# Kernel tuning notes

Hardware: AMD Instinct MI355X
Metric: run time of the kernel (lower is better)

Reference implementation:

```python
import jax, jax.numpy as jnp
import numpy as np

B, C, H, W = 32, 17, 96, 72
K = 3
DIL = 1
PAD = (K // 2) * DIL
KK = K * K


def setup_inputs() -> dict:
    key = jax.random.key(0)
    k1, k2, k3, k4, k5 = jax.random.split(key, 5)
    x = jax.random.normal(k1, (B, C, H, W), jnp.float32)
    offsets = jax.random.normal(k2, (B, 2 * C * KK, H, W), jnp.float32)
    mask = jax.random.uniform(k3, (B, C * KK, H, W), jnp.float32)
    # depthwise conv: weight [C_out=C, C_in/groups=1, K, K], bias [C]
    weight = jax.random.normal(k4, (C, 1, K, K), jnp.float32) * 0.1
    bias = jax.random.normal(k5, (C,), jnp.float32) * 0.01
    return {"x": x, "offsets": offsets, "mask": mask, "weight": weight, "bias": bias}


def _deform_conv(x, offsets, mask, weight, bias):
    # Modulated deformable conv (DCNv2), depthwise, offset_groups == channels.
    off = offsets.reshape(B, C, KK, 2, H, W)
    dy = off[:, :, :, 0]  # [B,C,KK,H,W]
    dx = off[:, :, :, 1]
    m = mask.reshape(B, C, KK, H, W)

    ky, kx = jnp.meshgrid(jnp.arange(K), jnp.arange(K), indexing="ij")
    ky = ky.reshape(KK)
    kx = kx.reshape(KK)
    hh = jnp.arange(H)
    ww = jnp.arange(W)
    # base sampling grid [KK,H,W]
    base_y = (-PAD + ky[:, None, None] * DIL + hh[None, :, None] + 0 * ww[None, None, :]).astype(jnp.float32)
    base_x = (-PAD + kx[:, None, None] * DIL + 0 * hh[None, :, None] + ww[None, None, :]).astype(jnp.float32)

    py = base_y[None, None] + dy  # [B,C,KK,H,W]
    px = base_x[None, None] + dx

    y0f = jnp.floor(py)
    x0f = jnp.floor(px)
    wy = py - y0f
    wx = px - x0f
    y0 = y0f.astype(jnp.int32)
    x0 = x0f.astype(jnp.int32)

    img = x.reshape(B, C, H * W)

    def corner(yi, xi, w):
        # zero-padding semantics: out-of-bounds corners contribute 0
        valid = (yi >= 0) & (yi < H) & (xi >= 0) & (xi < W)
        idx = jnp.clip(yi, 0, H - 1) * W + jnp.clip(xi, 0, W - 1)
        v = jnp.take_along_axis(img, idx.reshape(B, C, -1), axis=2).reshape(B, C, KK, H, W)
        return v * jnp.where(valid, w, 0.0)

    val = (corner(y0, x0, (1 - wy) * (1 - wx))
           + corner(y0, x0 + 1, (1 - wy) * wx)
           + corner(y0 + 1, x0, wy * (1 - wx))
           + corner(y0 + 1, x0 + 1, wy * wx))

    out = jnp.einsum("bckhw,ck->bchw", val * m, weight.reshape(C, KK))
    return out + bias[None, :, None, None]


def reference(x, offsets, mask, weight, bias):
    return _deform_conv(x, offsets, mask, weight, bias)
```

## Files before the change

kernel.cpp:

```cpp
#include <hip/hip_runtime.h>

#define Bn   32
#define Cn   17
#define Hn   96
#define Wn   72
#define Kn   3
#define KKn  9
#define PADn 1
#define HWn  (Hn * Wn)
#define TPB  576
#define ROWS_PER_BLOCK 32
#define NBLK_X (Hn / ROWS_PER_BLOCK)
#define NPX  4

#define PSTR 75
#define PROWS 99
#define XS_SIZE (PROWS * PSTR)

__global__ __launch_bounds__(TPB) void deform_conv_kernel(
    const float* __restrict__ x,
    const float* __restrict__ offsets,
    const float* __restrict__ mask,
    const float* __restrict__ weight,
    const float* __restrict__ bias,
    float* __restrict__ out)
{
    __shared__ float xs[XS_SIZE];

    const int tid = threadIdx.x;
    const int bc  = blockIdx.y;
    const int c   = bc % Cn;

    for (int i = tid; i < XS_SIZE; i += TPB) xs[i] = 0.f;
    __syncthreads();

    {
        const float4* __restrict__ xp4 = (const float4*)(x + (size_t)bc * HWn);
        #pragma unroll
        for (int j = 0; j < HWn / 4 / TPB; ++j) {
            const int ci  = j * TPB + tid;
            const float4 v = xp4[ci];
            const int idx = ci * 4;
            const int y = idx / Wn;
            const int xcol = idx - y * Wn;
            float* d = &xs[(y + 1) * PSTR + (xcol + 1)];
            d[0] = v.x; d[1] = v.y; d[2] = v.z; d[3] = v.w;
        }
    }
    __syncthreads();

    const int w  = tid % Wn;
    const int h0 = blockIdx.x * ROWS_PER_BLOCK + tid / Wn;
    const int hw0 = h0 * Wn + w;

    const float* __restrict__ offp = offsets + (size_t)bc * (KKn * 2 * HWn);
    const float* __restrict__ mp   = mask    + (size_t)bc * (KKn * HWn);
    const float* __restrict__ wp   = weight  + c * KKn;

    const float bv = bias[c];
    float acc[NPX] = {bv, bv, bv, bv};

    const float wf = (float)w;
    float hpf[NPX];
    #pragma unroll
    for (int p = 0; p < NPX; ++p) hpf[p] = (float)(h0 + 8 * p);

    #pragma unroll
    for (int kk = 0; kk < KKn; ++kk) {
        const float wk  = wp[kk];
        const int   ky  = kk / Kn;
        const int   kx  = kk - ky * Kn;
        const float kyo = (float)(ky - PADn);
        const float kxo = (float)(kx - PADn);

        float dyv[NPX], dxv[NPX], mv[NPX];
        #pragma unroll
        for (int p = 0; p < NPX; ++p) {
            const int hw_p = hw0 + p * 8 * Wn;
            dyv[p] = offp[(size_t)(kk * 2 + 0) * HWn + hw_p];
            dxv[p] = offp[(size_t)(kk * 2 + 1) * HWn + hw_p];
            mv[p]  = mp[(size_t)kk * HWn + hw_p];
        }

        #pragma unroll
        for (int p = 0; p < NPX; ++p) {
            float py = hpf[p] + (dyv[p] + kyo);
            float px = wf     + (dxv[p] + kxo);
            py = fminf(fmaxf(py, -1.f), (float)Hn);
            px = fminf(fmaxf(px, -1.f), (float)Wn);

            const float y0f = floorf(py);
            const float x0f = floorf(px);
            const float wy  = py - y0f;
            const float wx  = px - x0f;
            const int y0 = (int)y0f;
            const int x0 = (int)x0f;

            const float* pr = &xs[(y0 + 1) * PSTR + (x0 + 1)];
            const float v00 = pr[0];
            const float v01 = pr[1];
            const float v10 = pr[PSTR];
            const float v11 = pr[PSTR + 1];

            const float top = v00 + wx * (v01 - v00);
            const float bot = v10 + wx * (v11 - v10);
            const float v   = top + wy * (bot - top);

            acc[p] += v * (mv[p] * wk);
        }
    }

    const size_t ob = (size_t)bc * HWn;
    #pragma unroll
    for (int p = 0; p < NPX; ++p)
        out[ob + hw0 + p * 8 * Wn] = acc[p];
}

extern "C" void kernel_launch(void* const* d_in, const int* in_sizes, int n_in,
                              void* d_out, int out_size, void* d_ws, size_t ws_size,
                              hipStream_t stream) {
    const float* x       = (const float*)d_in[0];
    const float* offsets = (const float*)d_in[1];
    const float* mask    = (const float*)d_in[2];
    const float* weight  = (const float*)d_in[3];
    const float* bias    = (const float*)d_in[4];
    float* out = (float*)d_out;

    dim3 block(TPB, 1, 1);
    dim3 grid(NBLK_X, Bn * Cn, 1);
    deform_conv_kernel<<<grid, block, 0, stream>>>(x, offsets, mask, weight, bias, out);
}
```

Measured before the change: 449.3 us.

## Vectorize per-thread pixel loads with float4 nontemporal accesses and border-only zeroing

```diff
diff --git a/kernel.cpp b/kernel.cpp
--- a/kernel.cpp
+++ b/kernel.cpp
@@ -9,13 +9,15 @@
 #define PADn 1
 #define HWn  (Hn * Wn)
 #define TPB  576
-#define ROWS_PER_BLOCK 32
-#define NBLK_X (Hn / ROWS_PER_BLOCK)
 #define NPX  4
+#define CHUNK (TPB * NPX)
+#define NBLK_X (HWn / CHUNK)
 
 #define PSTR 75
 #define PROWS 99
 #define XS_SIZE (PROWS * PSTR)
+
+typedef float f4 __attribute__((ext_vector_type(4)));
 
 __global__ __launch_bounds__(TPB) void deform_conv_kernel(
     const float* __restrict__ x,
@@ -31,15 +33,23 @@
     const int bc  = blockIdx.y;
     const int c   = bc % Cn;
 
-    for (int i = tid; i < XS_SIZE; i += TPB) xs[i] = 0.f;
-    __syncthreads();
+    if (tid < 225) {
+        const int r  = (tid < 75) ? 0 : ((tid < 150) ? 97 : 98);
+        xs[r * PSTR + (tid % 75)] = 0.f;
+    } else if (tid < 513) {
+        const int i  = tid - 225;
+        const int r  = 1 + i / 3;
+        const int j  = i % 3;
+        const int cc = (j == 0) ? 0 : (72 + j);
+        xs[r * PSTR + cc] = 0.f;
+    }
 
     {
-        const float4* __restrict__ xp4 = (const float4*)(x + (size_t)bc * HWn);
+        const f4* __restrict__ xp4 = (const f4*)(x + (size_t)bc * HWn);
         #pragma unroll
         for (int j = 0; j < HWn / 4 / TPB; ++j) {
             const int ci  = j * TPB + tid;
-            const float4 v = xp4[ci];
+            const f4 v = xp4[ci];
             const int idx = ci * 4;
             const int y = idx / Wn;
             const int xcol = idx - y * Wn;
@@ -49,9 +59,9 @@
     }
     __syncthreads();
 
-    const int w  = tid % Wn;
-    const int h0 = blockIdx.x * ROWS_PER_BLOCK + tid / Wn;
-    const int hw0 = h0 * Wn + w;
+    const int hw0 = blockIdx.x * CHUNK + tid * NPX;
+    const int h   = hw0 / Wn;
+    const int w0  = hw0 - h * Wn;
 
     const float* __restrict__ offp = offsets + (size_t)bc * (KKn * 2 * HWn);
     const float* __restrict__ mp   = mask    + (size_t)bc * (KKn * HWn);
@@ -60,10 +70,8 @@
     const float bv = bias[c];
     float acc[NPX] = {bv, bv, bv, bv};
 
-    const float wf = (float)w;
-    float hpf[NPX];
-    #pragma unroll
-    for (int p = 0; p < NPX; ++p) hpf[p] = (float)(h0 + 8 * p);
+    const float hf  = (float)h;
+    const float wf0 = (float)w0;
 
     #pragma unroll
     for (int kk = 0; kk < KKn; ++kk) {
@@ -73,19 +81,23 @@
         const float kyo = (float)(ky - PADn);
         const float kxo = (float)(kx - PADn);
 
-        float dyv[NPX], dxv[NPX], mv[NPX];
-        #pragma unroll
-        for (int p = 0; p < NPX; ++p) {
-            const int hw_p = hw0 + p * 8 * Wn;
-            dyv[p] = offp[(size_t)(kk * 2 + 0) * HWn + hw_p];
-            dxv[p] = offp[(size_t)(kk * 2 + 1) * HWn + hw_p];
-            mv[p]  = mp[(size_t)kk * HWn + hw_p];
-        }
+        const f4 dy4 = __builtin_nontemporal_load(
+            (const f4*)(offp + (size_t)(kk * 2 + 0) * HWn + hw0));
+        const f4 dx4 = __builtin_nontemporal_load(
+            (const f4*)(offp + (size_t)(kk * 2 + 1) * HWn + hw0));
+        const f4 m4  = __builtin_nontemporal_load(
+            (const f4*)(mp + (size_t)kk * HWn + hw0));
+
+        const float dyv[NPX] = {dy4.x, dy4.y, dy4.z, dy4.w};
+        const float dxv[NPX] = {dx4.x, dx4.y, dx4.z, dx4.w};
+        const float mv [NPX] = {m4.x,  m4.y,  m4.z,  m4.w};
+
+        const float hk = hf + kyo;
 
         #pragma unroll
         for (int p = 0; p < NPX; ++p) {
-            float py = hpf[p] + (dyv[p] + kyo);
-            float px = wf     + (dxv[p] + kxo);
+            float py = hk + dyv[p];
+            float px = wf0 + ((float)p + kxo) + dxv[p];
             py = fminf(fmaxf(py, -1.f), (float)Hn);
             px = fminf(fmaxf(px, -1.f), (float)Wn);
 
@@ -110,10 +122,9 @@
         }
     }
 
-    const size_t ob = (size_t)bc * HWn;
-    #pragma unroll
-    for (int p = 0; p < NPX; ++p)
-        out[ob + hw0 + p * 8 * Wn] = acc[p];
+    f4 o;
+    o.x = acc[0]; o.y = acc[1]; o.z = acc[2]; o.w = acc[3];
+    __builtin_nontemporal_store(o, (f4*)(out + (size_t)bc * HWn + hw0));
 }
 
 extern "C" void kernel_launch(void* const* d_in, const int* in_sizes, int n_in,
```

Result: no change. 440.8 us (-1.9%).
